# Performance work log

Hardware: AMD Instinct MI355X
Metric: run time of the kernel (lower is better)

Reference implementation:

```python
import jax, jax.numpy as jnp
import numpy as np

NUM_GRAPHS = 512

def setup_inputs() -> dict:
    key = jax.random.key(0)
    ks = jax.random.split(key, 6)
    N, E, D = 100000, 1600000, 128
    x = jax.random.normal(ks[0], (N, D), dtype=jnp.float32)
    edge_index = jax.random.randint(ks[1], (2, E), 0, N, dtype=jnp.int64)
    batch = jnp.sort(jax.random.randint(ks[2], (N,), 0, NUM_GRAPHS, dtype=jnp.int64))
    scale = 1.0 / np.sqrt(D)
    Ws = jax.random.normal(ks[3], (4, D, D), dtype=jnp.float32) * scale
    bs = jnp.zeros((4, D), dtype=jnp.float32)
    Wl = jax.random.normal(ks[4], (D, 1), dtype=jnp.float32) * scale
    bl = jnp.zeros((1,), dtype=jnp.float32)
    return {"x": x, "edge_index": edge_index, "batch": batch,
            "Ws": Ws, "bs": bs, "Wl": Wl, "bl": bl}

def reference(x, edge_index, batch, Ws, bs, Wl, bl):
    N = x.shape[0]
    loops = jnp.arange(N, dtype=edge_index.dtype)
    # GCNConv: add self-loops, symmetric normalization D^{-1/2} A D^{-1/2}
    row = jnp.concatenate([edge_index[0], loops])  # source nodes
    col = jnp.concatenate([edge_index[1], loops])  # target nodes
    deg = jax.ops.segment_sum(jnp.ones_like(col, dtype=x.dtype), col, num_segments=N)
    dinv = jnp.where(deg > 0, jax.lax.rsqrt(jnp.maximum(deg, 1.0)), 0.0)
    norm = dinv[row] * dinv[col]  # [E+N]
    h = x
    for i in range(Ws.shape[0]):
        h = h @ Ws[i]                                   # [N, D]
        msg = h[row] * norm[:, None]                    # gather + scale, [E+N, D]
        h = jax.ops.segment_sum(msg, col, num_segments=N) + bs[i]
        h = jax.nn.relu(h)                              # dropout is identity in eval
    # global_mean_pool over graphs
    sums = jax.ops.segment_sum(h, batch, num_segments=NUM_GRAPHS)
    cnt = jax.ops.segment_sum(jnp.ones((N,), h.dtype), batch, num_segments=NUM_GRAPHS)
    pooled = sums / jnp.maximum(cnt, 1.0)[:, None]      # [G, D]
    return pooled @ Wl + bl                             # [G, 1]
```

## Files before the change

### kernel.cpp

```cpp
#include <hip/hip_runtime.h>


constexpr int D = 128;
constexpr int NGRAPH = 512;
constexpr int CHUNK = 4096;
constexpr int BSH = 9;
constexpr int OP = 136;

typedef __attribute__((ext_vector_type(8))) short bf16x8;
typedef __attribute__((ext_vector_type(4))) float f32x4;
typedef int i32x4u __attribute__((ext_vector_type(4), aligned(4)));

__device__ __forceinline__ float bf2f(unsigned short b) {
    return __uint_as_float(((unsigned int)b) << 16);
}
__device__ __forceinline__ unsigned short f2bf(float f) {
    unsigned int u = __float_as_uint(f);
    u += 0x7FFFu + ((u >> 16) & 1u);
    return (unsigned short)(u >> 16);
}

__global__ __launch_bounds__(256) void setup_all(
        const float4* __restrict__ x4, ushort4* __restrict__ hb, int n4, int CB,
        const float* __restrict__ W, unsigned short* __restrict__ Wt,
        const int* __restrict__ ec, int E, int* __restrict__ bucketCnt) {
    __shared__ int h[256];
    const int t = threadIdx.x;
    const int b = blockIdx.x;
    if (b < CB) {
        int i = b * 256 + t;
        if (i < n4) {
            float4 v = x4[i];
            ushort4 o;
            o.x = f2bf(v.x); o.y = f2bf(v.y); o.z = f2bf(v.z); o.w = f2bf(v.w);
            hb[i] = o;
        }
    } else if (b < CB + 256) {
        int idx = (b - CB) * 256 + t;
        int i = idx >> 14;
        int rem = idx & 16383;
        int k = rem >> 7, c = rem & 127;
        Wt[(i << 14) + c * 128 + k] = f2bf(W[idx]);
    } else {
        h[t] = 0;
        __syncthreads();
        const int e0 = (b - CB - 256) * CHUNK;
        const int cnt = min(CHUNK, E - e0);
        for (int i = t; i < cnt; i += 256) atomicAdd(&h[ec[e0 + i] >> BSH], 1);
        __syncthreads();
        if (h[t]) atomicAdd(&bucketCnt[t], h[t]);
    }
}

__global__ __launch_bounds__(256) void bucket_scan(const int* __restrict__ bucketCnt,
                                                   int* __restrict__ bucketBase,
                                                   int* __restrict__ globCursor) {
    __shared__ int s[256];
    const int t = threadIdx.x;
    int v = bucketCnt[t];
    s[t] = v; __syncthreads();
    for (int off = 1; off < 256; off <<= 1) {
        int x = (t >= off) ? s[t - off] : 0;
        __syncthreads();
        s[t] += x;
        __syncthreads();
    }
    int excl = s[t] - v;
    bucketBase[t] = excl;
    globCursor[t] = excl;
}

__global__ __launch_bounds__(256) void scatter_pairs(const int* __restrict__ er,
                                                     const int* __restrict__ ec, int E,
                                                     int* __restrict__ globCursor,
                                                     int2* __restrict__ pairs) {
    __shared__ int h[256], lbase[256], cur[256], segd[256], s[256];
    __shared__ int2 stage[CHUNK];
    const int t = threadIdx.x;
    const int e0 = blockIdx.x * CHUNK;
    const int cnt = min(CHUNK, E - e0);

    h[t] = 0;
    __syncthreads();
    for (int i = t; i < cnt; i += 256) atomicAdd(&h[ec[e0 + i] >> BSH], 1);
    __syncthreads();
    int v = h[t];
    s[t] = v; __syncthreads();
    for (int off = 1; off < 256; off <<= 1) {
        int x = (t >= off) ? s[t - off] : 0;
        __syncthreads();
        s[t] += x;
        __syncthreads();
    }
    lbase[t] = s[t] - v;
    cur[t] = s[t] - v;
    segd[t] = atomicAdd(&globCursor[t], v) - lbase[t];
    __syncthreads();
    for (int i = t; i < cnt; i += 256) {
        int c = ec[e0 + i];
        int b = c >> BSH;
        int p = atomicAdd(&cur[b], 1);
        stage[p] = make_int2(er[e0 + i], c);
    }
    __syncthreads();
    for (int i = t; i < cnt; i += 256) {
        int2 pr = stage[i];
        int b = pr.y >> BSH;
        pairs[segd[b] + i] = pr;
    }
}

__global__ __launch_bounds__(256) void fill_csr(const int2* __restrict__ pairs,
                                                const int* __restrict__ bucketBase,
                                                const int* __restrict__ bucketCnt,
                                                int N, int E, int NBUCK,
                                                int* __restrict__ rowptr,
                                                float* __restrict__ dinv,
                                                int* __restrict__ srcs) {
    __shared__ int hist[512], lofs[512], s[256];
    const int t = threadIdx.x;
    const int b = blockIdx.x;
    const int c0 = b << BSH;
    const int base = bucketBase[b];
    const int cnt = bucketCnt[b];
    const int2* pp = pairs + base;

    hist[t] = 0; hist[t + 256] = 0;
    __syncthreads();
    for (int i = t; i < cnt; i += 256) atomicAdd(&hist[pp[i].y - c0], 1);
    __syncthreads();
    int a0 = hist[2 * t], a1 = hist[2 * t + 1];
    s[t] = a0 + a1; __syncthreads();
    for (int off = 1; off < 256; off <<= 1) {
        int x = (t >= off) ? s[t - off] : 0;
        __syncthreads();
        s[t] += x;
        __syncthreads();
    }
    int excl = s[t] - (a0 + a1);
    lofs[2 * t] = excl;
    lofs[2 * t + 1] = excl + a0;
    __syncthreads();
    const int nn = min(512, N - c0);
    for (int i = t; i < nn; i += 256) {
        rowptr[c0 + i] = base + lofs[i];
        dinv[c0 + i] = rsqrtf((float)hist[i] + 1.0f);
    }
    if (b == NBUCK - 1 && t == 0) rowptr[N] = E;
    __syncthreads();
    for (int i = t; i < cnt; i += 256) {
        int2 pr = pp[i];
        int p = atomicAdd(&lofs[pr.y - c0], 1);
        srcs[base + p] = pr.x;
    }
}

__global__ __launch_bounds__(256) void scale_x(uint4* __restrict__ Hb0,
                                               const float* __restrict__ dinv,
                                               int nq) {
    int i = blockIdx.x * 256 + threadIdx.x;
    if (i >= nq) return;
    float dv = dinv[i >> 4];
    uint4 v = Hb0[i];
    unsigned int* p = (unsigned int*)&v;
#pragma unroll
    for (int k = 0; k < 4; ++k) {
        unsigned int d = p[k];
        unsigned short lo = f2bf(bf2f((unsigned short)(d & 0xFFFFu)) * dv);
        unsigned short hi = f2bf(bf2f((unsigned short)(d >> 16)) * dv);
        p[k] = ((unsigned int)hi << 16) | lo;
    }
    Hb0[i] = v;
}

__global__ __launch_bounds__(256, 4) void layer_fused(
        const int* __restrict__ rowptr, const int* __restrict__ srcs,
        const float* __restrict__ dinv, const unsigned short* __restrict__ H,
        const unsigned short* __restrict__ Wt, const float* __restrict__ bias,
        unsigned short* __restrict__ Hn, float* __restrict__ dots,
        const float* __restrict__ Wl, int N, int writeDots) {
    __shared__ __align__(16) unsigned short u[4][16 * OP];
    const int wave = threadIdx.x >> 6;
    const int lane = threadIdx.x & 63;
    const int row16 = lane & 15;
    const int quad = lane >> 4;
    const int r0 = blockIdx.x * 64 + wave * 16;
    unsigned short* U = u[wave];
    const bf16x8* H8 = (const bf16x8*)H;
    const int gl = row16;

#pragma unroll 1
    for (int sstep = 0; sstep < 4; ++sstep) {
        const int rt = quad * 4 + sstep;
        const int row = r0 + rt;
        float acc[8] = {0.f, 0.f, 0.f, 0.f, 0.f, 0.f, 0.f, 0.f};
        float sn = 0.f;
        if (row < N) {
            sn = dinv[row];
            int j = rowptr[row];
            const int end = rowptr[row + 1];
            bf16x8 hv = H8[(size_t)row * 16 + gl];
#pragma unroll
            for (int k = 0; k < 8; ++k) acc[k] = bf2f((unsigned short)hv[k]);
            const int ne = end - j;
            const int nb = (ne + 7) >> 3;
            if (nb > 0) {
                i32x4u sA0, sA1, sB0, sB1;
                {
                    const i32x4u* sp = (const i32x4u*)(srcs + j);
                    sA0 = sp[0]; sA1 = sp[1];
                }
                if (nb > 1) {
                    const i32x4u* sp = (const i32x4u*)(srcs + j + 8);
                    sB0 = sp[0]; sB1 = sp[1];
                }
                bf16x8 hc[8], hn[8];
#pragma unroll
                for (int t = 0; t < 8; ++t) {
                    int idx = (t < 4) ? sA0[t] : sA1[t - 4];
                    int rr = (t < ne) ? idx : row;
                    hc[t] = H8[(size_t)rr * 16 + gl];
                }
#pragma unroll 1
                for (int b = 0; b < nb; ++b) {
                    if (b + 1 < nb) {
                        const int remn = ne - (b + 1) * 8;
                        int rn[8];
#pragma unroll
                        for (int t = 0; t < 8; ++t) {
                            int idx = (t < 4) ? sB0[t] : sB1[t - 4];
                            rn[t] = (t < remn) ? idx : row;
                        }
                        if (b + 2 < nb) {
                            const i32x4u* sp = (const i32x4u*)(srcs + j + (b + 2) * 8);
                            sB0 = sp[0]; sB1 = sp[1];
                        }
#pragma unroll
                        for (int t = 0; t < 8; ++t)
                            hn[t] = H8[(size_t)rn[t] * 16 + gl];
                    }
                    const int rem = ne - b * 8;
#pragma unroll
                    for (int t = 0; t < 8; ++t) {
                        const float w = (t < rem) ? 1.f : 0.f;
#pragma unroll
                        for (int k = 0; k < 8; ++k)
                            acc[k] = fmaf(w, bf2f((unsigned short)hc[t][k]), acc[k]);
                    }
#pragma unroll
                    for (int t = 0; t < 8; ++t) hc[t] = hn[t];
                }
            }
        }
        bf16x8 o;
#pragma unroll
        for (int k = 0; k < 8; ++k) o[k] = (short)f2bf(sn * acc[k]);
        *(bf16x8*)(U + rt * 128 + ((gl ^ rt) << 3)) = o;
    }

    bf16x8 a0[4];
#pragma unroll
    for (int kc = 0; kc < 4; ++kc) {
        const int ph = (kc * 4 + quad) ^ row16;
        a0[kc] = *(const bf16x8*)(U + row16 * 128 + ph * 8);
    }

    float dv[4];
    if (!writeDots) {
#pragma unroll
        for (int i = 0; i < 4; ++i) {
            int ra = r0 + quad * 4 + i;
            dv[i] = (ra < N) ? dinv[ra] : 0.f;
        }
    }

    float rd[4] = {0.f, 0.f, 0.f, 0.f};
#pragma unroll
    for (int ct = 0; ct < 8; ++ct) {
        const int col = ct * 16 + row16;
        const bf16x8* wc = (const bf16x8*)(Wt + (size_t)col * 128);
        f32x4 acc0 = {0.f, 0.f, 0.f, 0.f};
#pragma unroll
        for (int kc = 0; kc < 4; ++kc) {
            const bf16x8 wf = wc[kc * 4 + quad];
            acc0 = __builtin_amdgcn_mfma_f32_16x16x32_bf16(a0[kc], wf, acc0, 0, 0, 0);
        }
        const float bv = bias[col];
        if (writeDots) {
            const float wl = Wl[col];
#pragma unroll
            for (int i = 0; i < 4; ++i) rd[i] += fmaxf(acc0[i] + bv, 0.f) * wl;
        } else {
#pragma unroll
            for (int i = 0; i < 4; ++i)
                U[(quad * 4 + i) * OP + col] = f2bf(dv[i] * fmaxf(acc0[i] + bv, 0.f));
        }
    }

    if (writeDots) {
#pragma unroll
        for (int m = 1; m < 16; m <<= 1)
#pragma unroll
            for (int i = 0; i < 4; ++i) rd[i] += __shfl_xor(rd[i], m, 64);
        if (row16 == 0) {
#pragma unroll
            for (int i = 0; i < 4; ++i) dots[r0 + quad * 4 + i] = rd[i];
        }
    } else {
#pragma unroll
        for (int i = 0; i < 4; ++i) {
            int idx = i * 64 + lane;
            int row = idx >> 4, c8 = idx & 15;
            bf16x8 v = *(const bf16x8*)(U + row * OP + c8 * 8);
            *(bf16x8*)(Hn + (size_t)(r0 + row) * 128 + c8 * 8) = v;
        }
    }
}

__global__ __launch_bounds__(256) void pool_graphs(const float* __restrict__ dots,
                                                   const int* __restrict__ batch, int N,
                                                   const float* __restrict__ bl,
                                                   float* __restrict__ out) {
    __shared__ int bounds[2];
    __shared__ float red[4];
    const int g = blockIdx.x;
    const int t = threadIdx.x;
    if (t < 2) {
        int key = g + t;
        int lo = 0, hi = N;
        while (lo < hi) {
            int mid = (lo + hi) >> 1;
            if (batch[mid] < key) lo = mid + 1; else hi = mid;
        }
        bounds[t] = lo;
    }
    __syncthreads();
    const int lo = bounds[0], hi = bounds[1];
    float s = 0.f;
    for (int i = lo + t; i < hi; i += 256) s += dots[i];
#pragma unroll
    for (int off = 32; off > 0; off >>= 1) s += __shfl_down(s, off, 64);
    if ((t & 63) == 0) red[t >> 6] = s;
    __syncthreads();
    if (t == 0) {
        float tot = red[0] + red[1] + red[2] + red[3];
        int cnt = hi - lo;
        out[g] = tot / (float)(cnt > 0 ? cnt : 1) + bl[0];
    }
}

extern "C" void kernel_launch(void* const* d_in, const int* in_sizes, int n_in,
                              void* d_out, int out_size, void* d_ws, size_t ws_size,
                              hipStream_t stream) {
    const float* x     = (const float*)d_in[0];
    const int*   eidx  = (const int*)d_in[1];
    const int*   batch = (const int*)d_in[2];
    const float* Ws    = (const float*)d_in[3];
    const float* bs    = (const float*)d_in[4];
    const float* Wl    = (const float*)d_in[5];
    const float* bl    = (const float*)d_in[6];
    (void)n_in; (void)out_size;

    const int N = in_sizes[0] / D;
    const int E = in_sizes[1] / 2;
    const int* er = eidx;
    const int* ec = eidx + E;
    const int NBUCK = (N + 511) >> BSH;
    const int NCHUNK = (E + CHUNK - 1) / CHUNK;

    const int Npad = (N + 127) & ~127;
    const size_t hBytes = (size_t)Npad * D * sizeof(unsigned short);
    auto al = [](size_t v) { return (v + 255) & ~(size_t)255; };
    char* base = (char*)d_ws;
    size_t off = 0;

    unsigned short* Hb0 = (unsigned short*)base; off = al(hBytes);
    int* bucketCnt  = (int*)(base + off);
    int* globCursor = bucketCnt + 256;
    off = al(off + 512 * sizeof(int));
    int*   bucketBase = (int*)(base + off);  off = al(off + 256 * sizeof(int));
    float* dinv   = (float*)(base + off);    off = al(off + (size_t)Npad * sizeof(float));
    float* dots   = (float*)(base + off);    off = al(off + (size_t)Npad * sizeof(float));
    int*   rowptr = (int*)(base + off);      off = al(off + (size_t)(Npad + 64) * sizeof(int));
    int*   srcs   = (int*)(base + off);      off = al(off + (size_t)E * sizeof(int) + 64);
    unsigned short* Wt = (unsigned short*)(base + off);   off = al(off + 4 * 128 * 128 * sizeof(unsigned short));

    const bool twoBuf = ws_size >= off + hBytes;
    unsigned short* Hb1 = twoBuf ? (unsigned short*)(base + off)
                                 : (unsigned short*)d_in[0];
    int2* pairs = (int2*)Hb1;
    unsigned short* hb[2] = { Hb0, Hb1 };

    hipMemsetAsync(bucketCnt, 0, 256 * sizeof(int), stream);
    const int n4 = N * D / 4;
    const int CB = (n4 + 255) / 256;
    setup_all<<<CB + 256 + NCHUNK, 256, 0, stream>>>((const float4*)x, (ushort4*)Hb0,
                                                     n4, CB, Ws, Wt, ec, E, bucketCnt);

    bucket_scan<<<1, 256, 0, stream>>>(bucketCnt, bucketBase, globCursor);
    scatter_pairs<<<NCHUNK, 256, 0, stream>>>(er, ec, E, globCursor, pairs);
    fill_csr<<<NBUCK, 256, 0, stream>>>(pairs, bucketBase, bucketCnt, N, E, NBUCK,
                                        rowptr, dinv, srcs);
    const int nq = N * 16;
    scale_x<<<(nq + 255) / 256, 256, 0, stream>>>((uint4*)Hb0, dinv, nq);

    for (int i = 0; i < 4; ++i) {
        const unsigned short* Hc = hb[i & 1];
        unsigned short* Hn = hb[(i + 1) & 1];
        layer_fused<<<Npad / 64, 256, 0, stream>>>(rowptr, srcs, dinv, Hc,
                                                   Wt + (size_t)i * D * D,
                                                   bs + (size_t)i * D, Hn, dots, Wl,
                                                   N, (i == 3) ? 1 : 0);
    }

    pool_graphs<<<NGRAPH, 256, 0, stream>>>(dots, batch, N, bl, (float*)d_out);
}
```

Measured before the change: 486.0 us.

## Pack CSR build pairs into single ints and split layer blocks across waves

The edge pairs used to build the CSR are packed into a single 32-bit int (source shifted left, low 9 bits for the target within its bucket), with the bucket id kept in a separate byte array. This halves the scatter and fill traffic, and CHUNK is halved to fit the new shared staging. The layer kernel now runs 128-thread blocks over 16 rows each: two waves share one aggregation tile and each computes half the output columns. The final-layer dot products are reduced across the two waves through shared memory. This gives more, smaller blocks and spreads the aggregation across more waves, but it adds block barriers and loads each 16-row A tile in both waves.

```diff
diff --git a/kernel.cpp b/kernel.cpp
--- a/kernel.cpp
+++ b/kernel.cpp
@@ -3,7 +3,7 @@
 
 constexpr int D = 128;
 constexpr int NGRAPH = 512;
-constexpr int CHUNK = 4096;
+constexpr int CHUNK = 2048;
 constexpr int BSH = 9;
 constexpr int OP = 136;
 
@@ -73,9 +73,10 @@
 __global__ __launch_bounds__(256) void scatter_pairs(const int* __restrict__ er,
                                                      const int* __restrict__ ec, int E,
                                                      int* __restrict__ globCursor,
-                                                     int2* __restrict__ pairs) {
+                                                     int* __restrict__ pairs) {
     __shared__ int h[256], lbase[256], cur[256], segd[256], s[256];
-    __shared__ int2 stage[CHUNK];
+    __shared__ int stage[CHUNK];
+    __shared__ unsigned char sb[CHUNK];
     const int t = threadIdx.x;
     const int e0 = blockIdx.x * CHUNK;
     const int cnt = min(CHUNK, E - e0);
@@ -100,17 +101,17 @@
         int c = ec[e0 + i];
         int b = c >> BSH;
         int p = atomicAdd(&cur[b], 1);
-        stage[p] = make_int2(er[e0 + i], c);
+        stage[p] = (er[e0 + i] << BSH) | (c & 511);
+        sb[p] = (unsigned char)b;
     }
     __syncthreads();
     for (int i = t; i < cnt; i += 256) {
-        int2 pr = stage[i];
-        int b = pr.y >> BSH;
-        pairs[segd[b] + i] = pr;
-    }
-}
-
-__global__ __launch_bounds__(256) void fill_csr(const int2* __restrict__ pairs,
+        int b = sb[i];
+        pairs[segd[b] + i] = stage[i];
+    }
+}
+
+__global__ __launch_bounds__(256) void fill_csr(const int* __restrict__ pairs,
                                                 const int* __restrict__ bucketBase,
                                                 const int* __restrict__ bucketCnt,
                                                 int N, int E, int NBUCK,
@@ -123,11 +124,11 @@
     const int c0 = b << BSH;
     const int base = bucketBase[b];
     const int cnt = bucketCnt[b];
-    const int2* pp = pairs + base;
+    const int* pp = pairs + base;
 
     hist[t] = 0; hist[t + 256] = 0;
     __syncthreads();
-    for (int i = t; i < cnt; i += 256) atomicAdd(&hist[pp[i].y - c0], 1);
+    for (int i = t; i < cnt; i += 256) atomicAdd(&hist[pp[i] & 511], 1);
     __syncthreads();
     int a0 = hist[2 * t], a1 = hist[2 * t + 1];
     s[t] = a0 + a1; __syncthreads();
@@ -149,9 +150,9 @@
     if (b == NBUCK - 1 && t == 0) rowptr[N] = E;
     __syncthreads();
     for (int i = t; i < cnt; i += 256) {
-        int2 pr = pp[i];
-        int p = atomicAdd(&lofs[pr.y - c0], 1);
-        srcs[base + p] = pr.x;
+        int pr = pp[i];
+        int p = atomicAdd(&lofs[pr & 511], 1);
+        srcs[base + p] = pr >> BSH;
     }
 }
 
@@ -173,25 +174,26 @@
     Hb0[i] = v;
 }
 
-__global__ __launch_bounds__(256, 4) void layer_fused(
+__global__ __launch_bounds__(128, 4) void layer_fused(
         const int* __restrict__ rowptr, const int* __restrict__ srcs,
         const float* __restrict__ dinv, const unsigned short* __restrict__ H,
         const unsigned short* __restrict__ Wt, const float* __restrict__ bias,
         unsigned short* __restrict__ Hn, float* __restrict__ dots,
         const float* __restrict__ Wl, int N, int writeDots) {
-    __shared__ __align__(16) unsigned short u[4][16 * OP];
-    const int wave = threadIdx.x >> 6;
-    const int lane = threadIdx.x & 63;
+    __shared__ __align__(16) unsigned short U[16 * OP];
+    const int tid = threadIdx.x;
+    const int wave = tid >> 6;
+    const int lane = tid & 63;
     const int row16 = lane & 15;
     const int quad = lane >> 4;
-    const int r0 = blockIdx.x * 64 + wave * 16;
-    unsigned short* U = u[wave];
+    const int grp = wave * 4 + quad;
+    const int r0 = blockIdx.x * 16;
     const bf16x8* H8 = (const bf16x8*)H;
     const int gl = row16;
 
 #pragma unroll 1
-    for (int sstep = 0; sstep < 4; ++sstep) {
-        const int rt = quad * 4 + sstep;
+    for (int ss = 0; ss < 2; ++ss) {
+        const int rt = grp * 2 + ss;
         const int row = r0 + rt;
         float acc[8] = {0.f, 0.f, 0.f, 0.f, 0.f, 0.f, 0.f, 0.f};
         float sn = 0.f;
@@ -257,6 +259,7 @@
         for (int k = 0; k < 8; ++k) o[k] = (short)f2bf(sn * acc[k]);
         *(bf16x8*)(U + rt * 128 + ((gl ^ rt) << 3)) = o;
     }
+    __syncthreads();
 
     bf16x8 a0[4];
 #pragma unroll
@@ -264,6 +267,7 @@
         const int ph = (kc * 4 + quad) ^ row16;
         a0[kc] = *(const bf16x8*)(U + row16 * 128 + ph * 8);
     }
+    __syncthreads();
 
     float dv[4];
     if (!writeDots) {
@@ -276,7 +280,8 @@
 
     float rd[4] = {0.f, 0.f, 0.f, 0.f};
 #pragma unroll
-    for (int ct = 0; ct < 8; ++ct) {
+    for (int c = 0; c < 4; ++c) {
+        const int ct = wave * 4 + c;
         const int col = ct * 16 + row16;
         const bf16x8* wc = (const bf16x8*)(Wt + (size_t)col * 128);
         f32x4 acc0 = {0.f, 0.f, 0.f, 0.f};
@@ -302,14 +307,18 @@
         for (int m = 1; m < 16; m <<= 1)
 #pragma unroll
             for (int i = 0; i < 4; ++i) rd[i] += __shfl_xor(rd[i], m, 64);
+        float* R = (float*)U;
         if (row16 == 0) {
 #pragma unroll
-            for (int i = 0; i < 4; ++i) dots[r0 + quad * 4 + i] = rd[i];
-        }
+            for (int i = 0; i < 4; ++i) R[wave * 16 + quad * 4 + i] = rd[i];
+        }
+        __syncthreads();
+        if (tid < 16) dots[r0 + tid] = R[tid] + R[16 + tid];
     } else {
-#pragma unroll
-        for (int i = 0; i < 4; ++i) {
-            int idx = i * 64 + lane;
+        __syncthreads();
+#pragma unroll
+        for (int i = 0; i < 2; ++i) {
+            int idx = i * 128 + tid;
             int row = idx >> 4, c8 = idx & 15;
             bf16x8 v = *(const bf16x8*)(U + row * OP + c8 * 8);
             *(bf16x8*)(Hn + (size_t)(r0 + row) * 128 + c8 * 8) = v;
@@ -382,13 +391,13 @@
     float* dinv   = (float*)(base + off);    off = al(off + (size_t)Npad * sizeof(float));
     float* dots   = (float*)(base + off);    off = al(off + (size_t)Npad * sizeof(float));
     int*   rowptr = (int*)(base + off);      off = al(off + (size_t)(Npad + 64) * sizeof(int));
-    int*   srcs   = (int*)(base + off);      off = al(off + (size_t)E * sizeof(int) + 64);
+    int*   srcs   = (int*)(base + off);      off = al(off + ((size_t)E + 64) * sizeof(int));
     unsigned short* Wt = (unsigned short*)(base + off);   off = al(off + 4 * 128 * 128 * sizeof(unsigned short));
 
     const bool twoBuf = ws_size >= off + hBytes;
     unsigned short* Hb1 = twoBuf ? (unsigned short*)(base + off)
                                  : (unsigned short*)d_in[0];
-    int2* pairs = (int2*)Hb1;
+    int* pairs = (int*)Hb1;
     unsigned short* hb[2] = { Hb0, Hb1 };
 
     hipMemsetAsync(bucketCnt, 0, 256 * sizeof(int), stream);
@@ -407,7 +416,7 @@
     for (int i = 0; i < 4; ++i) {
         const unsigned short* Hc = hb[i & 1];
         unsigned short* Hn = hb[(i + 1) & 1];
-        layer_fused<<<Npad / 64, 256, 0, stream>>>(rowptr, srcs, dinv, Hc,
+        layer_fused<<<Npad / 16, 128, 0, stream>>>(rowptr, srcs, dinv, Hc,
                                                    Wt + (size_t)i * D * D,
                                                    bs + (size_t)i * D, Hn, dots, Wl,
                                                    N, (i == 3) ? 1 : 0);
```

Result: faster. 466.9 us (-3.9%).
